# Optimization experiments

Hardware: AMD Instinct MI355X
Metric: run time of the kernel (lower is better)

Reference implementation:

```python
import jax, jax.numpy as jnp
import numpy as np

B, IN, H = 8192, 1024, 2048

def setup_inputs() -> dict:
    key = jax.random.key(0)
    k1, k2, k3, k4, k5 = jax.random.split(key, 5)
    prev_state = jax.random.normal(k1, (B, H), dtype=jnp.float32)
    x = jax.random.normal(k2, (B, IN), dtype=jnp.float32)
    input_weights = jax.random.normal(k3, (H, IN), dtype=jnp.float32) / IN ** 0.5
    input_bias = jnp.zeros((H,), dtype=jnp.float32)
    recurrent_weights = jax.random.normal(k4, (H, H), dtype=jnp.float32) / H ** 0.5
    U_z = jax.random.normal(k5, (H, H), dtype=jnp.float32) / H ** 0.5
    b_u = jnp.zeros((H,), dtype=jnp.float32)
    return {"prev_state": prev_state, "input": x,
            "input_weights": input_weights, "input_bias": input_bias,
            "recurrent_weights": recurrent_weights, "U_z": U_z, "b_u": b_u}

def reference(prev_state, input, input_weights, input_bias, recurrent_weights, U_z, b_u):
    # z = tanh(x @ W_x^T + b_x)
    z = jnp.tanh(input @ input_weights.T + input_bias)
    # u = sigmoid(h @ W_h^T + z @ U_z^T + b_u)
    u = jax.nn.sigmoid(prev_state @ recurrent_weights.T + z @ U_z.T + b_u)
    # convex combination of previous state and candidate
    state = u * prev_state + (1.0 - u) * z
    return state
```

## Files before the change

kernel.cpp:

```cpp
#include <hip/hip_runtime.h>
#include <hip/hip_bf16.h>
#include <cstdint>
#include <cstddef>

#define DEVFN static __device__ __forceinline__

typedef __attribute__((ext_vector_type(8))) short bf16x8;
typedef __attribute__((ext_vector_type(4))) float f32x4;

static constexpr int kB = 8192;
static constexpr int kIN = 1024;
static constexpr int kH = 2048;

DEVFN unsigned short f32_to_bf16(float f) {
  union { float f; unsigned int u; } v; v.f = f;
  unsigned int x = v.u;
  x += 0x7fffu + ((x >> 16) & 1u);
  return (unsigned short)(x >> 16);
}
DEVFN float bf16_to_f32(unsigned short u) {
  union { unsigned int u; float f; } v; v.u = (unsigned int)u << 16;
  return v.f;
}

__global__ void cast_all(const float* __restrict__ x, const float* __restrict__ Wx,
                         const float* __restrict__ Wh, const float* __restrict__ Uz,
                         const float* __restrict__ h,
                         unsigned short* __restrict__ xb, unsigned short* __restrict__ Wxb,
                         unsigned short* __restrict__ Wcat, unsigned short* __restrict__ Acat) {
  const long i = (long)blockIdx.x * blockDim.x + threadIdx.x;
  const float* src; unsigned short* dst; int sh, stride, off; long li;
  if (i < 2097152L)      { li = i;            src = x;  dst = xb;   sh = 8; stride = 1024; off = 0; }
  else if (i < 2621440L) { li = i - 2097152L; src = Wx; dst = Wxb;  sh = 8; stride = 1024; off = 0; }
  else if (i < 3670016L) { li = i - 2621440L; src = Wh; dst = Wcat; sh = 9; stride = 4096; off = 0; }
  else if (i < 4718592L) { li = i - 3670016L; src = Uz; dst = Wcat; sh = 9; stride = 4096; off = 2048; }
  else                   { li = i - 4718592L; src = h;  dst = Acat; sh = 9; stride = 4096; off = 0; }
  float4 v = *(const float4*)(src + li * 4);
  const long row = li >> sh;
  const long col = (li & ((1L << sh) - 1)) * 4;
  unsigned short* d = dst + row * stride + off + col;
  ushort4 o;
  o.x = f32_to_bf16(v.x); o.y = f32_to_bf16(v.y);
  o.z = f32_to_bf16(v.z); o.w = f32_to_bf16(v.w);
  *(ushort4*)d = o;
}

typedef const __attribute__((address_space(1))) unsigned int* gptr_t;
typedef __attribute__((address_space(3))) unsigned int* lptr_t;
DEVFN void gload16(const unsigned short* g, unsigned short* l) {
  __builtin_amdgcn_global_load_lds((gptr_t)g, (lptr_t)l, 16, 0, 0);
}

DEVFN void bar() { __builtin_amdgcn_s_barrier(); }
#define VMC0() asm volatile("s_waitcnt vmcnt(0)" ::: "memory")
#define VMC2() asm volatile("s_waitcnt vmcnt(2)" ::: "memory")


template<int BUF, int QM, int MI0, int MI1>
DEVFN void ldA(bf16x8 (&a)[4][2], const unsigned short* LA0, const unsigned short* LA1) {
#pragma unroll
  for (int mi = MI0; mi < MI1; ++mi) {
    a[mi][0] = *(const bf16x8*)(LA0 + BUF * 16384 + QM * 4096 + mi * 1024);
    a[mi][1] = *(const bf16x8*)(LA1 + BUF * 16384 + QM * 4096 + mi * 1024);
  }
}

template<int BUF, int QN>
DEVFN void ldB(bf16x8 (&b)[4][2], const unsigned short* LB0, const unsigned short* LB1) {
#pragma unroll
  for (int ni = 0; ni < 2; ++ni) {
    const int n = QN * 2 + ni;
    b[n][0] = *(const bf16x8*)(LB0 + BUF * 16384 + n * 1024);
    b[n][1] = *(const bf16x8*)(LB1 + BUF * 16384 + n * 1024);
  }
}

template<int QM, int QN>
DEVFN void mfmaQ(f32x4 (&acc)[8][4], bf16x8 (&a)[4][2], bf16x8 (&b)[4][2]) {
  __builtin_amdgcn_s_setprio(1);
#pragma unroll
  for (int kk = 0; kk < 2; ++kk)
#pragma unroll
    for (int mi = 0; mi < 4; ++mi)
#pragma unroll
      for (int ni = 0; ni < 2; ++ni)
        acc[QM * 4 + mi][QN * 2 + ni] = __builtin_amdgcn_mfma_f32_16x16x32_bf16(
            a[mi][kk], b[QN * 2 + ni][kk], acc[QM * 4 + mi][QN * 2 + ni], 0, 0, 0);
  __builtin_amdgcn_s_setprio(0);
}

template<int EPI>
__global__ __launch_bounds__(512, 1)
void gemm256(const unsigned short* __restrict__ A,
             const unsigned short* __restrict__ W,
             const float* __restrict__ bias,
             int M, int K,
             unsigned short* __restrict__ zOut,
             const unsigned short* __restrict__ hzBuf, int ldhz,
             float* __restrict__ out, int ldo)
{
  __shared__ unsigned short lds[8][8192];
  unsigned short* L = &lds[0][0];

  const int nTM = M >> 8;
  const int bm = blockIdx.x % nTM, bn = blockIdx.x / nTM;
  const int rowBase = bm << 8, colBase = bn << 8;

  const int t = threadIdx.x;
  const int l = t & 63;
  const int w = t >> 6;
  const int lr = l & 15, lg = l >> 4;
  const int wm = w >> 2, wn = w & 3;

  const int kel0 = (lg * 8) ^ ((lr & 7) * 8);
  const unsigned short* LA0 = L + wm * 8192 + lr * 64 + kel0;
  const unsigned short* LA1 = L + wm * 8192 + lr * 64 + (kel0 ^ 32);
  const unsigned short* LB0 = L + 32768 + (wn >> 1) * 8192 + (wn & 1) * 4096 + lr * 64 + kel0;
  const unsigned short* LB1 = L + 32768 + (wn >> 1) * 8192 + (wn & 1) * 4096 + lr * 64 + (kel0 ^ 32);

  const int srow = t >> 3;
  const int scol = (t & 7) * 8;
  const int kcSrc = scol ^ ((srow & 7) * 8);
  const unsigned short* pa0 = A + (size_t)(rowBase + srow) * K + kcSrc;
  const unsigned short* pa1 = pa0 + (size_t)64 * K;
  const unsigned short* pa2 = pa0 + (size_t)128 * K;
  const unsigned short* pa3 = pa0 + (size_t)192 * K;
  const unsigned short* pb0 = W + (size_t)(colBase + srow) * K + kcSrc;
  const unsigned short* pb1 = pb0 + (size_t)64 * K;
  const unsigned short* pb2 = pb0 + (size_t)128 * K;
  const unsigned short* pb3 = pb0 + (size_t)192 * K;

  unsigned short* const sd = L + w * 512;
#define STAGE(P0, P1, BUF, OP, HALF, OFSE) do {                                \
    unsigned short* ld = sd + (OP) * 32768 + ((BUF) * 2 + (HALF)) * 8192;      \
    gload16((P0) + (OFSE), ld);                                                \
    gload16((P1) + (OFSE), ld + 4096);                                         \
  } while (0)

  f32x4 acc[8][4] = {};
  bf16x8 a[4][2], b[4][2];

  STAGE(pa0, pa1, 0, 0, 0, 0);  STAGE(pa2, pa3, 0, 0, 1, 0);
  STAGE(pb0, pb1, 0, 1, 0, 0);  STAGE(pb2, pb3, 0, 1, 1, 0);
  STAGE(pb0, pb1, 1, 1, 0, 64); STAGE(pb2, pb3, 1, 1, 1, 64);
  STAGE(pa0, pa1, 1, 0, 0, 64); STAGE(pa2, pa3, 1, 0, 1, 64);
  VMC0();
  bar();
  ldA<0, 0, 0, 2>(a, LA0, LA1);
  ldB<0, 0>(b, LB0, LB1);

  const int NP = K >> 7;
  for (int j = 0; j < NP - 1; ++j) {
    ldA<0, 0, 2, 4>(a, LA0, LA1);
    ldB<0, 1>(b, LB0, LB1);
    STAGE(pa2, pa3, 1, 0, 1, 64);
    bar();
    mfmaQ<0, 0>(acc, a, b);
    bar();
    bar();
    mfmaQ<0, 1>(acc, a, b);
    ldA<0, 1, 0, 4>(a, LA0, LA1);
    bar();
    STAGE(pb0, pb1, 0, 1, 0, 128);
    bar();
    mfmaQ<1, 0>(acc, a, b);
    VMC2();
    bar();
    ldB<1, 0>(b, LB0, LB1);
    STAGE(pb2, pb3, 0, 1, 1, 128);
    bar();
    mfmaQ<1, 1>(acc, a, b);
    ldA<1, 0, 0, 2>(a, LA0, LA1);
    bar();
    ldA<1, 0, 2, 4>(a, LA0, LA1);
    ldB<1, 1>(b, LB0, LB1);
    STAGE(pa0, pa1, 0, 0, 0, 128);
    bar();
    mfmaQ<0, 0>(acc, a, b);
    bar();
    STAGE(pa2, pa3, 0, 0, 1, 128);
    bar();
    mfmaQ<0, 1>(acc, a, b);
    ldA<1, 1, 0, 4>(a, LA0, LA1);
    bar();
    STAGE(pb0, pb1, 1, 1, 0, 192);
    bar();
    mfmaQ<1, 0>(acc, a, b);
    VMC2();
    bar();
    ldB<0, 0>(b, LB0, LB1);
    STAGE(pb2, pb3, 1, 1, 1, 192);
    STAGE(pa0, pa1, 1, 0, 0, 192);
    bar();
    mfmaQ<1, 1>(acc, a, b);
    ldA<0, 0, 0, 2>(a, LA0, LA1);
    bar();
    pa0 += 128; pa1 += 128; pa2 += 128; pa3 += 128;
    pb0 += 128; pb1 += 128; pb2 += 128; pb3 += 128;
  }
  {
    ldA<0, 0, 2, 4>(a, LA0, LA1);
    ldB<0, 1>(b, LB0, LB1);
    STAGE(pa2, pa3, 1, 0, 1, 64);
    bar();
    mfmaQ<0, 0>(acc, a, b);
    bar();
    bar();
    mfmaQ<0, 1>(acc, a, b);
    ldA<0, 1, 0, 4>(a, LA0, LA1);
    bar();
    bar();
    mfmaQ<1, 0>(acc, a, b);
    VMC0();
    bar();
    ldB<1, 0>(b, LB0, LB1);
    bar();
    mfmaQ<1, 1>(acc, a, b);
    ldA<1, 0, 0, 2>(a, LA0, LA1);
    bar();
    ldA<1, 0, 2, 4>(a, LA0, LA1);
    ldB<1, 1>(b, LB0, LB1);
    bar();
    mfmaQ<0, 0>(acc, a, b);
    bar();
    bar();
    mfmaQ<0, 1>(acc, a, b);
    ldA<1, 1, 0, 4>(a, LA0, LA1);
    bar();
    bar();
    mfmaQ<1, 0>(acc, a, b);
    bar();
    bar();
    mfmaQ<1, 1>(acc, a, b);
    bar();
  }
#undef STAGE

  if (EPI == 0) {
    unsigned short* Z = L;
#pragma unroll
    for (int m = 0; m < 8; ++m) {
      const int rl = wm * 128 + m * 16 + lg * 4;
#pragma unroll
      for (int n = 0; n < 4; ++n) {
        const int cl = wn * 64 + n * 16 + lr;
        const float bs = bias[colBase + cl];
#pragma unroll
        for (int q = 0; q < 4; ++q) {
          const int r = rl + q;
          const int sc = cl ^ ((r & 7) * 8);
          Z[r * 256 + sc] = f32_to_bf16(tanhf(acc[m][n][q] + bs));
        }
      }
    }
    bar();
#pragma unroll
    for (int s = 0; s < 16; ++s) {
      const int gofs = (s * 512 + t) * 8;
      const int row = gofs >> 8;
      const int c0 = gofs & 255;
      const int sc0 = c0 ^ ((row & 7) * 8);
      bf16x8 v = *(const bf16x8*)(Z + row * 256 + sc0);
      *(bf16x8*)(zOut + (size_t)(rowBase + row) * ldhz + colBase + c0) = v;
    }
  } else {
#pragma unroll
    for (int m = 0; m < 8; ++m) {
      const int r0 = rowBase + wm * 128 + m * 16 + lg * 4;
#pragma unroll
      for (int n = 0; n < 4; ++n) {
        const int c = colBase + wn * 64 + n * 16 + lr;
        const float bs = bias[c];
#pragma unroll
        for (int q = 0; q < 4; ++q) {
          const int r = r0 + q;
          const float pre = acc[m][n][q] + bs;
          const float u = 1.0f / (1.0f + __expf(-pre));
          const float hv = bf16_to_f32(hzBuf[(size_t)r * ldhz + c]);
          const float zv = bf16_to_f32(hzBuf[(size_t)r * ldhz + 2048 + c]);
          out[(size_t)r * ldo + c] = u * hv + (1.0f - u) * zv;
        }
      }
    }
  }
}

extern "C" void kernel_launch(void* const* d_in, const int* in_sizes, int n_in,
                              void* d_out, int out_size, void* d_ws, size_t ws_size,
                              hipStream_t stream) {
  const float* h  = (const float*)d_in[0];
  const float* x  = (const float*)d_in[1];
  const float* Wx = (const float*)d_in[2];
  const float* bx = (const float*)d_in[3];
  const float* Wh = (const float*)d_in[4];
  const float* Uz = (const float*)d_in[5];
  const float* bu = (const float*)d_in[6];
  float* out = (float*)d_out;

  unsigned short* ws   = (unsigned short*)d_ws;
  unsigned short* xb   = ws;
  unsigned short* Wxb  = xb + (size_t)kB * kIN;
  unsigned short* Wcat = Wxb + (size_t)kH * kIN;
  unsigned short* Acat = Wcat + (size_t)kH * 2 * kH;

  cast_all<<<34816, 256, 0, stream>>>(x, Wx, Wh, Uz, h, xb, Wxb, Wcat, Acat);

  const int grid = (kB / 256) * (kH / 256);

  gemm256<0><<<grid, 512, 0, stream>>>(
      xb, Wxb, bx, kB, kIN, Acat + kH, nullptr, 2 * kH, nullptr, 0);

  gemm256<1><<<grid, 512, 0, stream>>>(
      Acat, Wcat, bu, kB, 2 * kH, nullptr, Acat, 2 * kH, out, kH);
}
```

Measured before the change: 211.9 us.

## Hold full B tile in registers and reschedule global-to-LDS staging

Each k-step now loads the whole B fragment into one of two register sets, alternating between even and odd sets, instead of reloading half of B per quadrant. This frees the LDS B buffer early so the next B tile can be staged sooner. The order of the global-to-LDS copies is reworked, with waitcnt thresholds raised to 6 and 4 so more loads stay in flight. The cost is more VGPR pressure from the second B register set and a riskier synchronisation schedule.

```diff
diff --git a/kernel.cpp b/kernel.cpp
--- a/kernel.cpp
+++ b/kernel.cpp
@@ -53,7 +53,8 @@
 
 DEVFN void bar() { __builtin_amdgcn_s_barrier(); }
 #define VMC0() asm volatile("s_waitcnt vmcnt(0)" ::: "memory")
-#define VMC2() asm volatile("s_waitcnt vmcnt(2)" ::: "memory")
+#define VMC4() asm volatile("s_waitcnt vmcnt(4)" ::: "memory")
+#define VMC6() asm volatile("s_waitcnt vmcnt(6)" ::: "memory")
 
 
 template<int BUF, int QM, int MI0, int MI1>
@@ -65,18 +66,14 @@
   }
 }
 
-template<int BUF, int QN>
-DEVFN void ldB(bf16x8 (&b)[4][2], const unsigned short* LB0, const unsigned short* LB1) {
-#pragma unroll
-  for (int ni = 0; ni < 2; ++ni) {
-    const int n = QN * 2 + ni;
-    b[n][0] = *(const bf16x8*)(LB0 + BUF * 16384 + n * 1024);
-    b[n][1] = *(const bf16x8*)(LB1 + BUF * 16384 + n * 1024);
-  }
+template<int BUF, int N>
+DEVFN void ldB1(bf16x8 (&bx)[4][2], const unsigned short* LB0, const unsigned short* LB1) {
+  bx[N][0] = *(const bf16x8*)(LB0 + BUF * 16384 + N * 1024);
+  bx[N][1] = *(const bf16x8*)(LB1 + BUF * 16384 + N * 1024);
 }
 
 template<int QM, int QN>
-DEVFN void mfmaQ(f32x4 (&acc)[8][4], bf16x8 (&a)[4][2], bf16x8 (&b)[4][2]) {
+DEVFN void mfmaQ(f32x4 (&acc)[8][4], bf16x8 (&a)[4][2], bf16x8 (&bx)[4][2]) {
   __builtin_amdgcn_s_setprio(1);
 #pragma unroll
   for (int kk = 0; kk < 2; ++kk)
@@ -85,7 +82,7 @@
 #pragma unroll
       for (int ni = 0; ni < 2; ++ni)
         acc[QM * 4 + mi][QN * 2 + ni] = __builtin_amdgcn_mfma_f32_16x16x32_bf16(
-            a[mi][kk], b[QN * 2 + ni][kk], acc[QM * 4 + mi][QN * 2 + ni], 0, 0, 0);
+            a[mi][kk], bx[QN * 2 + ni][kk], acc[QM * 4 + mi][QN * 2 + ni], 0, 0, 0);
   __builtin_amdgcn_s_setprio(0);
 }
 
@@ -138,61 +135,68 @@
   } while (0)
 
   f32x4 acc[8][4] = {};
-  bf16x8 a[4][2], b[4][2];
-
+  bf16x8 a[4][2], bE[4][2], bO[4][2];
+
+  STAGE(pb0, pb1, 0, 1, 0, 0);  STAGE(pb2, pb3, 0, 1, 1, 0);
   STAGE(pa0, pa1, 0, 0, 0, 0);  STAGE(pa2, pa3, 0, 0, 1, 0);
-  STAGE(pb0, pb1, 0, 1, 0, 0);  STAGE(pb2, pb3, 0, 1, 1, 0);
   STAGE(pb0, pb1, 1, 1, 0, 64); STAGE(pb2, pb3, 1, 1, 1, 64);
   STAGE(pa0, pa1, 1, 0, 0, 64); STAGE(pa2, pa3, 1, 0, 1, 64);
   VMC0();
   bar();
   ldA<0, 0, 0, 2>(a, LA0, LA1);
-  ldB<0, 0>(b, LB0, LB1);
+  ldB1<0, 0>(bE, LB0, LB1); ldB1<0, 1>(bE, LB0, LB1);
+  ldB1<0, 2>(bE, LB0, LB1); ldB1<0, 3>(bE, LB0, LB1);
 
   const int NP = K >> 7;
   for (int j = 0; j < NP - 1; ++j) {
     ldA<0, 0, 2, 4>(a, LA0, LA1);
-    ldB<0, 1>(b, LB0, LB1);
-    STAGE(pa2, pa3, 1, 0, 1, 64);
-    bar();
-    mfmaQ<0, 0>(acc, a, b);
-    bar();
-    bar();
-    mfmaQ<0, 1>(acc, a, b);
+    ldB1<1, 0>(bO, LB0, LB1);
+    STAGE(pb0, pb1, 0, 1, 0, 128);
+    bar();
+    mfmaQ<0, 0>(acc, a, bE);
+    bar();
+    ldB1<1, 1>(bO, LB0, LB1);
+    STAGE(pb2, pb3, 0, 1, 1, 128);
+    bar();
+    mfmaQ<0, 1>(acc, a, bE);
     ldA<0, 1, 0, 4>(a, LA0, LA1);
     bar();
-    STAGE(pb0, pb1, 0, 1, 0, 128);
-    bar();
-    mfmaQ<1, 0>(acc, a, b);
-    VMC2();
-    bar();
-    ldB<1, 0>(b, LB0, LB1);
-    STAGE(pb2, pb3, 0, 1, 1, 128);
-    bar();
-    mfmaQ<1, 1>(acc, a, b);
+    ldB1<1, 2>(bO, LB0, LB1);
+    STAGE(pa0, pa1, 0, 0, 0, 128);
+    bar();
+    mfmaQ<1, 0>(acc, a, bE);
+    VMC6();
+    bar();
+    ldB1<1, 3>(bO, LB0, LB1);
+    STAGE(pa2, pa3, 0, 0, 1, 128);
+    bar();
+    mfmaQ<1, 1>(acc, a, bE);
+    VMC4();
     ldA<1, 0, 0, 2>(a, LA0, LA1);
     bar();
     ldA<1, 0, 2, 4>(a, LA0, LA1);
-    ldB<1, 1>(b, LB0, LB1);
-    STAGE(pa0, pa1, 0, 0, 0, 128);
-    bar();
-    mfmaQ<0, 0>(acc, a, b);
-    bar();
-    STAGE(pa2, pa3, 0, 0, 1, 128);
-    bar();
-    mfmaQ<0, 1>(acc, a, b);
+    ldB1<0, 0>(bE, LB0, LB1);
+    STAGE(pb0, pb1, 1, 1, 0, 192);
+    bar();
+    mfmaQ<0, 0>(acc, a, bO);
+    bar();
+    ldB1<0, 1>(bE, LB0, LB1);
+    STAGE(pb2, pb3, 1, 1, 1, 192);
+    bar();
+    mfmaQ<0, 1>(acc, a, bO);
     ldA<1, 1, 0, 4>(a, LA0, LA1);
     bar();
-    STAGE(pb0, pb1, 1, 1, 0, 192);
-    bar();
-    mfmaQ<1, 0>(acc, a, b);
-    VMC2();
-    bar();
-    ldB<0, 0>(b, LB0, LB1);
-    STAGE(pb2, pb3, 1, 1, 1, 192);
+    ldB1<0, 2>(bE, LB0, LB1);
     STAGE(pa0, pa1, 1, 0, 0, 192);
     bar();
-    mfmaQ<1, 1>(acc, a, b);
+    mfmaQ<1, 0>(acc, a, bO);
+    VMC6();
+    bar();
+    ldB1<0, 3>(bE, LB0, LB1);
+    STAGE(pa2, pa3, 1, 0, 1, 192);
+    bar();
+    mfmaQ<1, 1>(acc, a, bO);
+    VMC4();
     ldA<0, 0, 0, 2>(a, LA0, LA1);
     bar();
     pa0 += 128; pa1 += 128; pa2 += 128; pa3 += 128;
@@ -200,38 +204,38 @@
   }
   {
     ldA<0, 0, 2, 4>(a, LA0, LA1);
-    ldB<0, 1>(b, LB0, LB1);
-    STAGE(pa2, pa3, 1, 0, 1, 64);
-    bar();
-    mfmaQ<0, 0>(acc, a, b);
-    bar();
-    bar();
-    mfmaQ<0, 1>(acc, a, b);
+    ldB1<1, 0>(bO, LB0, LB1);
+    bar();
+    mfmaQ<0, 0>(acc, a, bE);
+    bar();
+    ldB1<1, 1>(bO, LB0, LB1);
+    bar();
+    mfmaQ<0, 1>(acc, a, bE);
     ldA<0, 1, 0, 4>(a, LA0, LA1);
     bar();
-    bar();
-    mfmaQ<1, 0>(acc, a, b);
+    ldB1<1, 2>(bO, LB0, LB1);
+    bar();
+    mfmaQ<1, 0>(acc, a, bE);
     VMC0();
     bar();
-    ldB<1, 0>(b, LB0, LB1);
-    bar();
-    mfmaQ<1, 1>(acc, a, b);
+    ldB1<1, 3>(bO, LB0, LB1);
+    bar();
+    mfmaQ<1, 1>(acc, a, bE);
     ldA<1, 0, 0, 2>(a, LA0, LA1);
     bar();
     ldA<1, 0, 2, 4>(a, LA0, LA1);
-    ldB<1, 1>(b, LB0, LB1);
-    bar();
-    mfmaQ<0, 0>(acc, a, b);
-    bar();
-    bar();
-    mfmaQ<0, 1>(acc, a, b);
+    bar();
+    mfmaQ<0, 0>(acc, a, bO);
+    bar();
+    bar();
+    mfmaQ<0, 1>(acc, a, bO);
     ldA<1, 1, 0, 4>(a, LA0, LA1);
     bar();
     bar();
-    mfmaQ<1, 0>(acc, a, b);
-    bar();
-    bar();
-    mfmaQ<1, 1>(acc, a, b);
+    mfmaQ<1, 0>(acc, a, bO);
+    bar();
+    bar();
+    mfmaQ<1, 1>(acc, a, bO);
     bar();
   }
 #undef STAGE
```

After: 375.2 us. 77.1% more time.
